# Performance work log

Measured on AMD Instinct MI355X. Metric: run time of the kernel, lower is better.

Reference implementation:

```python
import jax, jax.numpy as jnp
import numpy as np

A = -0.75  # cubic convolution coefficient used by PyTorch bicubic


def cubic_weights(t):
    """t: fractional offset in [0,1). Returns (4, *t.shape) weights for taps at
    floor-1, floor, floor+1, floor+2 (Keys cubic convolution, a=-0.75)."""
    t2 = t * t
    s = 1.0 - t
    w1 = (A + 2.0) * t * t2 - (A + 3.0) * t2 + 1.0          # dist = t
    w2 = (A + 2.0) * s * s * s - (A + 3.0) * s * s + 1.0     # dist = 1-t
    u = 1.0 + t
    w0 = A * (u * (u * (u - 5.0) + 8.0) - 4.0)               # dist = 1+t
    v = 2.0 - t
    w3 = A * (v * (v * (v - 5.0) + 8.0) - 4.0)               # dist = 2-t
    return jnp.stack([w0, w1, w2, w3])


def _resize_last(x, n_out):
    """Bicubic 1D resize along the last axis, align_corners=True, border-clamped
    access (matches F.interpolate(mode='bicubic', align_corners=True))."""
    n_in = x.shape[-1]
    if n_in == n_out:
        return x
    src = jnp.arange(n_out, dtype=x.dtype) * ((n_in - 1) / (n_out - 1))
    i0 = jnp.floor(src).astype(jnp.int32)
    t = src - i0.astype(x.dtype)
    w = cubic_weights(t)  # (4, n_out)
    out = jnp.zeros(x.shape[:-1] + (n_out,), x.dtype)
    for k in range(4):
        idx = jnp.clip(i0 - 1 + k, 0, n_in - 1)
        out = out + jnp.take(x, idx, axis=-1) * w[k]
    return out


def bicubic_resize(x, h_out, w_out):
    """x: (b, h, w, c) -> (b, h_out, w_out, c); separable, align_corners=True."""
    x = jnp.moveaxis(_resize_last(jnp.moveaxis(x, 1, -1), h_out), -1, 1)
    x = jnp.moveaxis(_resize_last(jnp.moveaxis(x, 2, -1), w_out), -1, 2)
    return x


def grid_sample_bicubic_zeros(img, gx, gy):
    """img: (b,H,W); gx,gy: (b,h,w) normalized coords in [-1,1].
    Matches F.grid_sample(mode='bicubic', padding_mode='zeros', align_corners=True)."""
    b, H, W = img.shape
    ix = (gx + 1.0) * 0.5 * (W - 1)
    iy = (gy + 1.0) * 0.5 * (H - 1)
    ix0 = jnp.floor(ix)
    iy0 = jnp.floor(iy)
    wx = cubic_weights(ix - ix0)  # (4,b,h,w)
    wy = cubic_weights(iy - iy0)
    ix0 = ix0.astype(jnp.int32)
    iy0 = iy0.astype(jnp.int32)
    b_idx = jnp.arange(b)[:, None, None]
    out = jnp.zeros(gx.shape, img.dtype)
    for i in range(4):
        yy = iy0 - 1 + i
        ymask = (yy >= 0) & (yy < H)
        yc = jnp.clip(yy, 0, H - 1)
        for j in range(4):
            xx = ix0 - 1 + j
            mask = ymask & (xx >= 0) & (xx < W)
            xc = jnp.clip(xx, 0, W - 1)
            v = img[b_idx, yc, xc]
            out = out + wy[i] * wx[j] * jnp.where(mask, v, 0.0)
    return out


def setup_inputs() -> dict:
    key = jax.random.key(0)
    k1, k2 = jax.random.split(key)
    B = 8
    PH, PW = 1024, 1024
    CH, CW = 16, 16
    input_phantom = jax.random.normal(k1, (B, 1, PH, PW), dtype=jnp.float32)
    # learned warp control points; small shifts like a trained model would have
    shiftmap = jax.random.normal(k2, (B, CH, CW, 2), dtype=jnp.float32) * 0.05
    # mesh buffer: meshgrid('ij') of linspace(-1,1,PH) x linspace(-1,1,PW), stacked last
    ys = jnp.linspace(-1.0, 1.0, PH, dtype=jnp.float32)
    xs = jnp.linspace(-1.0, 1.0, PW, dtype=jnp.float32)
    my, mx = jnp.meshgrid(ys, xs, indexing='ij')
    mesh = jnp.stack([my, mx], axis=-1)[None]  # (1, PH, PW, 2)
    return {"input_phantom": input_phantom, "shiftmap": shiftmap, "mesh": mesh}


def reference(input_phantom, shiftmap, mesh):
    b, _, H, W = input_phantom.shape
    ph, pw = mesh.shape[1], mesh.shape[2]
    ch, cw = shiftmap.shape[1], shiftmap.shape[2]
    trans = (ch == 1 and cw == 1)
    if (not trans) and (ch != ph or cw != pw):
        sm = bicubic_resize(shiftmap, ph, pw)  # (b, ph, pw, 2)
    else:
        sm = shiftmap
    shift_mesh = mesh + sm  # broadcast to (b, ph, pw, 2); channel 0 = y, 1 = x
    # .flip(-1) means grid x = channel 1, grid y = channel 0
    gx = shift_mesh[..., 1]
    gy = shift_mesh[..., 0]
    warped = grid_sample_bicubic_zeros(input_phantom[:, 0], gx, gy)
    return warped[:, None]  # (b, 1, ph, pw)
```

## Files before the change

### kernel.cpp

```cpp
#include <hip/hip_runtime.h>


static constexpr float A = -0.75f;
static constexpr int NXCD = 8;

__device__ __forceinline__ void cubic_weights(float t, float* w) {
    float t2 = t * t;
    float s  = 1.0f - t;
    w[1] = (A + 2.0f) * t * t2 - (A + 3.0f) * t2 + 1.0f;
    w[2] = (A + 2.0f) * s * s * s - (A + 3.0f) * s * s + 1.0f;
    float u = 1.0f + t;
    w[0] = A * (u * (u * (u - 5.0f) + 8.0f) - 4.0f);
    float v = 2.0f - t;
    w[3] = A * (v * (v * (v - 5.0f) + 8.0f) - 4.0f);
}

template <int PX_PER_THREAD>
__global__ __launch_bounds__(256) void shiftmap_warp_kernel(
    const float* __restrict__ img,
    const float* __restrict__ smap,
    float* __restrict__ out,
    int H, int W, int CH, int CW, int nblocks)
{
    const int d   = blockIdx.x;
    const int per = nblocks / NXCD;
    const int work = (d % NXCD) * per + d / NXCD;
    const int y = work % H;
    const int b = work / H;
    const int tid = threadIdx.x;

    __shared__ float s_row[64];

    const float scale_y = (float)((double)(CH - 1) / (double)(H - 1));
    const float scale_x = (float)((double)(CW - 1) / (double)(W - 1));

    if (tid < CW * 2) {
        const int c  = tid >> 1;
        const int ch = tid & 1;
        const float sy  = y * scale_y;
        const float fy0 = floorf(sy);
        const int   cy0 = (int)fy0;
        float wy[4];
        cubic_weights(sy - fy0, wy);
        float v = 0.0f;
        #pragma unroll
        for (int i = 0; i < 4; ++i) {
            const int cy = min(max(cy0 - 1 + i, 0), CH - 1);
            v += wy[i] * smap[(((size_t)b * CH + cy) * CW + c) * 2 + ch];
        }
        s_row[tid] = v;
    }
    __syncthreads();

    const float half_w = 0.5f * (float)(W - 1);
    const float half_h = 0.5f * (float)(H - 1);
    const float* imgb = img + (size_t)b * H * W;
    float* outb = out + (size_t)b * H * W + (size_t)y * W;

    #pragma unroll
    for (int k = 0; k < PX_PER_THREAD; ++k) {
        const int x = tid + k * 256;

        const float sx  = x * scale_x;
        const float fx0 = floorf(sx);
        const int   cx0 = (int)fx0;
        float wx[4];
        cubic_weights(sx - fx0, wx);
        float smy = 0.0f, smx = 0.0f;
        #pragma unroll
        for (int j = 0; j < 4; ++j) {
            const int cx = min(max(cx0 - 1 + j, 0), CW - 1);
            smy += wx[j] * s_row[cx * 2 + 0];
            smx += wx[j] * s_row[cx * 2 + 1];
        }

        const float ix = (float)x + smx * half_w;
        const float iy = (float)y + smy * half_h;
        const float ixf = floorf(ix), iyf = floorf(iy);
        const int ix0 = (int)ixf, iy0 = (int)iyf;
        float gwx[4], gwy[4];
        cubic_weights(ix - ixf, gwx);
        cubic_weights(iy - iyf, gwy);

        float acc = 0.0f;
        if (ix0 >= 1 && ix0 <= W - 3 && iy0 >= 1 && iy0 <= H - 3) {
            const float* p = imgb + (size_t)(iy0 - 1) * W + (ix0 - 1);
            #pragma unroll
            for (int i = 0; i < 4; ++i) {
                const float r = gwx[0] * p[0] + gwx[1] * p[1]
                              + gwx[2] * p[2] + gwx[3] * p[3];
                acc += gwy[i] * r;
                p += W;
            }
        } else {
            #pragma unroll
            for (int i = 0; i < 4; ++i) {
                const int yy = iy0 - 1 + i;
                const bool vy = (yy >= 0) && (yy < H);
                const int yc = min(max(yy, 0), H - 1);
                const float* row = imgb + (size_t)yc * W;
                float r = 0.0f;
                #pragma unroll
                for (int j = 0; j < 4; ++j) {
                    const int xx = ix0 - 1 + j;
                    const bool v = vy && (xx >= 0) && (xx < W);
                    const int xc = min(max(xx, 0), W - 1);
                    r += gwx[j] * (v ? row[xc] : 0.0f);
                }
                acc += gwy[i] * r;
            }
        }
        outb[x] = acc;
    }
}

extern "C" void kernel_launch(void* const* d_in, const int* in_sizes, int n_in,
                              void* d_out, int out_size, void* d_ws, size_t ws_size,
                              hipStream_t stream) {
    const float* img  = (const float*)d_in[0];
    const float* smap = (const float*)d_in[1];
    float* out = (float*)d_out;

    const int H = 1024, W = 1024;
    const int CH = 16, CW = 16;
    const int B = in_sizes[0] / (H * W);
    const int nblocks = H * B;

    dim3 block(256);
    dim3 grid(nblocks);
    shiftmap_warp_kernel<4><<<grid, block, 0, stream>>>(img, smap, out, H, W, CH, CW, nblocks);
}
```

Baseline: 47.90 us.

## Precompute x-direction shiftmap interpolation in a separate kernel via workspace

Adds a small pre-pass kernel that bicubically interpolates the coarse shiftmap along x for every coarse row and output column, pre-scaled by half-width and half-height, and stores the result as float2 in the workspace. The main warp kernel then only does the y interpolation from four precomputed rows. This removes the per-pixel x-weight computation, the shared-memory stage and the __syncthreads. The interior tap loads are also grouped ahead of the FMAs to expose memory parallelism. In exchange it adds a second kernel launch and extra global reads of the precomputed rows, and keeps the old kernel as a fallback when the workspace is too small.

```diff
diff --git a/kernel.cpp b/kernel.cpp
--- a/kernel.cpp
+++ b/kernel.cpp
@@ -15,45 +15,57 @@
     w[3] = A * (v * (v * (v - 5.0f) + 8.0f) - 4.0f);
 }
 
+__global__ __launch_bounds__(256) void xinterp_kernel(
+    const float* __restrict__ smap,
+    float2* __restrict__ xsc,
+    int W, int CH, int CW, float scale_x, float half_h, float half_w)
+{
+    const int x  = blockIdx.x * 256 + threadIdx.x;
+    const int cy = blockIdx.y;
+    const int b  = blockIdx.z;
+    if (x >= W) return;
+
+    const float sx  = x * scale_x;
+    const float fx0 = floorf(sx);
+    const int   cx0 = (int)fx0;
+    float wx[4];
+    cubic_weights(sx - fx0, wx);
+
+    const float* row = smap + (((size_t)b * CH + cy) * CW) * 2;
+    float vy = 0.0f, vx = 0.0f;
+    #pragma unroll
+    for (int j = 0; j < 4; ++j) {
+        const int cx = min(max(cx0 - 1 + j, 0), CW - 1);
+        vy += wx[j] * row[cx * 2 + 0];
+        vx += wx[j] * row[cx * 2 + 1];
+    }
+    xsc[((size_t)b * CH + cy) * W + x] = make_float2(vy * half_h, vx * half_w);
+}
+
 template <int PX_PER_THREAD>
 __global__ __launch_bounds__(256) void shiftmap_warp_kernel(
     const float* __restrict__ img,
-    const float* __restrict__ smap,
+    const float2* __restrict__ xsc,
     float* __restrict__ out,
-    int H, int W, int CH, int CW, int nblocks)
+    int H, int W, int CH, int nblocks, float scale_y)
 {
-    const int d   = blockIdx.x;
-    const int per = nblocks / NXCD;
+    const int d    = blockIdx.x;
+    const int per  = nblocks / NXCD;
     const int work = (d % NXCD) * per + d / NXCD;
     const int y = work % H;
     const int b = work / H;
     const int tid = threadIdx.x;
 
-    __shared__ float s_row[64];
-
-    const float scale_y = (float)((double)(CH - 1) / (double)(H - 1));
-    const float scale_x = (float)((double)(CW - 1) / (double)(W - 1));
-
-    if (tid < CW * 2) {
-        const int c  = tid >> 1;
-        const int ch = tid & 1;
-        const float sy  = y * scale_y;
-        const float fy0 = floorf(sy);
-        const int   cy0 = (int)fy0;
-        float wy[4];
-        cubic_weights(sy - fy0, wy);
-        float v = 0.0f;
-        #pragma unroll
-        for (int i = 0; i < 4; ++i) {
-            const int cy = min(max(cy0 - 1 + i, 0), CH - 1);
-            v += wy[i] * smap[(((size_t)b * CH + cy) * CW + c) * 2 + ch];
-        }
-        s_row[tid] = v;
-    }
-    __syncthreads();
-
-    const float half_w = 0.5f * (float)(W - 1);
-    const float half_h = 0.5f * (float)(H - 1);
+    const float sy  = y * scale_y;
+    const float fy0 = floorf(sy);
+    const int   cy0 = (int)fy0;
+    float wy[4];
+    cubic_weights(sy - fy0, wy);
+    const float2* bp0 = xsc + ((size_t)b * CH + min(max(cy0 - 1, 0), CH - 1)) * W;
+    const float2* bp1 = xsc + ((size_t)b * CH + min(max(cy0    , 0), CH - 1)) * W;
+    const float2* bp2 = xsc + ((size_t)b * CH + min(max(cy0 + 1, 0), CH - 1)) * W;
+    const float2* bp3 = xsc + ((size_t)b * CH + min(max(cy0 + 2, 0), CH - 1)) * W;
+
     const float* imgb = img + (size_t)b * H * W;
     float* outb = out + (size_t)b * H * W + (size_t)y * W;
 
@@ -61,21 +73,12 @@
     for (int k = 0; k < PX_PER_THREAD; ++k) {
         const int x = tid + k * 256;
 
-        const float sx  = x * scale_x;
-        const float fx0 = floorf(sx);
-        const int   cx0 = (int)fx0;
-        float wx[4];
-        cubic_weights(sx - fx0, wx);
-        float smy = 0.0f, smx = 0.0f;
-        #pragma unroll
-        for (int j = 0; j < 4; ++j) {
-            const int cx = min(max(cx0 - 1 + j, 0), CW - 1);
-            smy += wx[j] * s_row[cx * 2 + 0];
-            smx += wx[j] * s_row[cx * 2 + 1];
-        }
-
-        const float ix = (float)x + smx * half_w;
-        const float iy = (float)y + smy * half_h;
+        const float2 c0 = bp0[x], c1 = bp1[x], c2 = bp2[x], c3 = bp3[x];
+        const float smy = wy[0] * c0.x + wy[1] * c1.x + wy[2] * c2.x + wy[3] * c3.x;
+        const float smx = wy[0] * c0.y + wy[1] * c1.y + wy[2] * c2.y + wy[3] * c3.y;
+
+        const float ix = (float)x + smx;
+        const float iy = (float)y + smy;
         const float ixf = floorf(ix), iyf = floorf(iy);
         const int ix0 = (int)ixf, iy0 = (int)iyf;
         float gwx[4], gwy[4];
@@ -85,12 +88,16 @@
         float acc = 0.0f;
         if (ix0 >= 1 && ix0 <= W - 3 && iy0 >= 1 && iy0 <= H - 3) {
             const float* p = imgb + (size_t)(iy0 - 1) * W + (ix0 - 1);
+            float f[4][4];
             #pragma unroll
             for (int i = 0; i < 4; ++i) {
-                const float r = gwx[0] * p[0] + gwx[1] * p[1]
-                              + gwx[2] * p[2] + gwx[3] * p[3];
-                acc += gwy[i] * r;
+                f[i][0] = p[0]; f[i][1] = p[1]; f[i][2] = p[2]; f[i][3] = p[3];
                 p += W;
+            }
+            #pragma unroll
+            for (int i = 0; i < 4; ++i) {
+                acc += gwy[i] * (gwx[0] * f[i][0] + gwx[1] * f[i][1]
+                               + gwx[2] * f[i][2] + gwx[3] * f[i][3]);
             }
         } else {
             #pragma unroll
@@ -114,6 +121,87 @@
     }
 }
 
+template <int PX_PER_THREAD>
+__global__ __launch_bounds__(256) void shiftmap_warp_fallback(
+    const float* __restrict__ img, const float* __restrict__ smap,
+    float* __restrict__ out, int H, int W, int CH, int CW, int nblocks)
+{
+    const int d   = blockIdx.x;
+    const int per = nblocks / NXCD;
+    const int work = (d % NXCD) * per + d / NXCD;
+    const int y = work % H;
+    const int b = work / H;
+    const int tid = threadIdx.x;
+
+    __shared__ float s_row[64];
+    const float scale_y = (float)((double)(CH - 1) / (double)(H - 1));
+    const float scale_x = (float)((double)(CW - 1) / (double)(W - 1));
+
+    if (tid < CW * 2) {
+        const int c = tid >> 1, ch = tid & 1;
+        const float sy = y * scale_y;
+        const float fy0 = floorf(sy);
+        const int cy0 = (int)fy0;
+        float wy[4];
+        cubic_weights(sy - fy0, wy);
+        float v = 0.0f;
+        #pragma unroll
+        for (int i = 0; i < 4; ++i) {
+            const int cy = min(max(cy0 - 1 + i, 0), CH - 1);
+            v += wy[i] * smap[(((size_t)b * CH + cy) * CW + c) * 2 + ch];
+        }
+        s_row[tid] = v;
+    }
+    __syncthreads();
+
+    const float half_w = 0.5f * (float)(W - 1);
+    const float half_h = 0.5f * (float)(H - 1);
+    const float* imgb = img + (size_t)b * H * W;
+    float* outb = out + (size_t)b * H * W + (size_t)y * W;
+
+    #pragma unroll
+    for (int k = 0; k < PX_PER_THREAD; ++k) {
+        const int x = tid + k * 256;
+        const float sx = x * scale_x;
+        const float fx0 = floorf(sx);
+        const int cx0 = (int)fx0;
+        float wx[4];
+        cubic_weights(sx - fx0, wx);
+        float smy = 0.0f, smx = 0.0f;
+        #pragma unroll
+        for (int j = 0; j < 4; ++j) {
+            const int cx = min(max(cx0 - 1 + j, 0), CW - 1);
+            smy += wx[j] * s_row[cx * 2 + 0];
+            smx += wx[j] * s_row[cx * 2 + 1];
+        }
+        const float ix = (float)x + smx * half_w;
+        const float iy = (float)y + smy * half_h;
+        const float ixf = floorf(ix), iyf = floorf(iy);
+        const int ix0 = (int)ixf, iy0 = (int)iyf;
+        float gwx[4], gwy[4];
+        cubic_weights(ix - ixf, gwx);
+        cubic_weights(iy - iyf, gwy);
+        float acc = 0.0f;
+        #pragma unroll
+        for (int i = 0; i < 4; ++i) {
+            const int yy = iy0 - 1 + i;
+            const bool vy = (yy >= 0) && (yy < H);
+            const int yc = min(max(yy, 0), H - 1);
+            const float* row = imgb + (size_t)yc * W;
+            float r = 0.0f;
+            #pragma unroll
+            for (int j = 0; j < 4; ++j) {
+                const int xx = ix0 - 1 + j;
+                const bool v = vy && (xx >= 0) && (xx < W);
+                const int xc = min(max(xx, 0), W - 1);
+                r += gwx[j] * (v ? row[xc] : 0.0f);
+            }
+            acc += gwy[i] * r;
+        }
+        outb[x] = acc;
+    }
+}
+
 extern "C" void kernel_launch(void* const* d_in, const int* in_sizes, int n_in,
                               void* d_out, int out_size, void* d_ws, size_t ws_size,
                               hipStream_t stream) {
@@ -126,7 +214,23 @@
     const int B = in_sizes[0] / (H * W);
     const int nblocks = H * B;
 
-    dim3 block(256);
-    dim3 grid(nblocks);
-    shiftmap_warp_kernel<4><<<grid, block, 0, stream>>>(img, smap, out, H, W, CH, CW, nblocks);
-}
+    const float scale_y = (float)((double)(CH - 1) / (double)(H - 1));
+    const float scale_x = (float)((double)(CW - 1) / (double)(W - 1));
+    const float half_h = 0.5f * (float)(H - 1);
+    const float half_w = 0.5f * (float)(W - 1);
+
+    const size_t ws_needed = (size_t)B * CH * W * sizeof(float2);
+    if (ws_size >= ws_needed) {
+        float2* xsc = (float2*)d_ws;
+        dim3 g1(W / 256, CH, B);
+        xinterp_kernel<<<g1, 256, 0, stream>>>(smap, xsc, W, CH, CW,
+                                               scale_x, half_h, half_w);
+        dim3 g2(nblocks);
+        shiftmap_warp_kernel<4><<<g2, 256, 0, stream>>>(img, xsc, out,
+                                                        H, W, CH, nblocks, scale_y);
+    } else {
+        dim3 g2(nblocks);
+        shiftmap_warp_fallback<4><<<g2, 256, 0, stream>>>(img, smap, out,
+                                                          H, W, CH, CW, nblocks);
+    }
+}
```

Result: slower. 66.16 us (+38.1%).
